# Performance work log

Measured on AMD Instinct MI355X. Metric: run time of the kernel, lower is better.

## Reference

```python
import jax, jax.numpy as jnp
import numpy as np

K = 64        # top-k from init_kwargs
TAU = 1.0     # temperature at step=0: tau_start*(1-0) + tau_end*0


def setup_inputs() -> dict:
    key = jax.random.key(0)
    k1, k2 = jax.random.split(key)
    B, N = 2048, 8192
    logits = jax.random.normal(k1, (B, N), dtype=jnp.float32)
    # gumbels = -log(Exp(1)) == standard Gumbel noise
    gumbel_noise = jax.random.gumbel(k2, (B, N), dtype=jnp.float32)
    return {"logits": logits, "gumbel_noise": gumbel_noise}


def reference(logits, gumbel_noise):
    # training path of GumbelTopK (step=0 -> tau=TAU, hard=True)
    g = (logits + gumbel_noise) / TAU                       # [B, N]
    order = jnp.argsort(-g, axis=-1)                        # descending sort order
    sorted_g = jnp.take_along_axis(g, order, axis=-1)
    cumsum = jnp.cumsum(jax.nn.softmax(sorted_g, axis=-1), axis=-1)
    mask = (cumsum <= K).astype(sorted_g.dtype)             # NB: faithful to source (<= k)
    sorted_y = mask * jax.nn.softmax(sorted_g / TAU, axis=-1)
    # scatter back to original positions == gather by inverse permutation
    inv = jnp.argsort(order, axis=-1)
    y = jnp.take_along_axis(sorted_y, inv, axis=-1)         # [B, N]
    # hard straight-through: one-hot-k of y
    k = min(K, y.shape[-1])
    _, idx = jax.lax.top_k(y, k)                            # [B, k]
    rows = jnp.arange(y.shape[0])[:, None]
    y_hard = jnp.zeros_like(y).at[rows, idx].set(1.0)
    return jax.lax.stop_gradient(y_hard - y) + y
```

## Files before the change

### kernel.cpp

```cpp
#include <hip/hip_runtime.h>

constexpr int N = 8192;
constexpr int K = 64;
constexpr int THREADS = 512;
constexpr int WAVES = THREADS / 64;
constexpr int EPT = N / THREADS;
constexpr int VEC = EPT / 4;
constexpr int CAP = 3072;

typedef float f32x4 __attribute__((ext_vector_type(4)));

__device__ __forceinline__ unsigned orderable(float f) {
    unsigned x = __float_as_uint(f);
    return (x & 0x80000000u) ? ~x : (x | 0x80000000u);
}

__global__ __launch_bounds__(THREADS, 8)
void gumbel_topk_onehot(const float* __restrict__ logits,
                        const float* __restrict__ noise,
                        float* __restrict__ out)
{
    __shared__ __align__(16) unsigned hist[2048];
    __shared__ __align__(16) unsigned cand[CAP];
    __shared__ unsigned wavesum[WAVES];
    __shared__ unsigned ccount;
    __shared__ unsigned sel_bin, sel_kth, sel_cnt;
    __shared__ unsigned r_val, r_take, r_ceq;

    const int tid  = threadIdx.x;
    const int lane = tid & 63;
    const int wave = tid >> 6;
    const long long row = blockIdx.x;

    const float4* lrow = (const float4*)(logits + row * (long long)N);
    const float4* nrow = (const float4*)(noise  + row * (long long)N);

    ((uint4*)hist)[tid] = make_uint4(0, 0, 0, 0);
    if (tid == 0) ccount = 0;

    unsigned key[EPT];
#pragma unroll
    for (int i = 0; i < VEC; ++i) {
        int idx = tid + i * THREADS;
        float4 a = lrow[idx];
        float4 b = nrow[idx];
        key[4*i+0] = orderable(a.x + b.x);
        key[4*i+1] = orderable(a.y + b.y);
        key[4*i+2] = orderable(a.z + b.z);
        key[4*i+3] = orderable(a.w + b.w);
    }
    __syncthreads();

#pragma unroll
    for (int e = 0; e < EPT; ++e)
        atomicAdd(&hist[key[e] >> 21], 1u);
    __syncthreads();

    unsigned kth = K;

#define SELECT_BIN(BPT)                                                      \
    {                                                                        \
        unsigned p = 0;                                                      \
        _Pragma("unroll")                                                    \
        for (int j = 0; j < (BPT); ++j) p += hist[tid * (BPT) + j];          \
        unsigned s = p;                                                      \
        _Pragma("unroll")                                                    \
        for (int off = 1; off < 64; off <<= 1) {                             \
            unsigned v = __shfl_down(s, off);                                \
            if (lane + off < 64) s += v;                                     \
        }                                                                    \
        if (lane == 0) wavesum[wave] = s;                                    \
        __syncthreads();                                                     \
        unsigned S = s;                                                      \
        _Pragma("unroll")                                                    \
        for (int w = 0; w < WAVES; ++w) if (w > wave) S += wavesum[w];       \
        unsigned Snext = S - p;                                              \
        if (S >= kth && Snext < kth) {                                       \
            unsigned cum = Snext;                                            \
            for (int j = (BPT) - 1; j >= 0; --j) {                           \
                unsigned c = hist[tid * (BPT) + j];                          \
                if (cum + c >= kth) {                                        \
                    sel_bin = (unsigned)(tid * (BPT) + j);                   \
                    sel_kth = kth - cum;                                     \
                    sel_cnt = c;                                             \
                    break;                                                   \
                }                                                            \
                cum += c;                                                    \
            }                                                                \
        }                                                                    \
        __syncthreads();                                                     \
    }

    SELECT_BIN(4)
    const unsigned b1   = sel_bin;
    const unsigned cnt1 = sel_cnt;
    kth = sel_kth;

#pragma unroll
    for (int e = 0; e < EPT; ++e) {
        if ((key[e] >> 21) == b1) {
            unsigned pos = atomicAdd(&ccount, 1u);
            if (pos < (unsigned)CAP) cand[pos] = key[e] & 0x1FFFFFu;
        }
    }
    __syncthreads();

    unsigned T, take_eq, c_eq;

    if (cnt1 <= (unsigned)THREADS) {
        const bool have = (tid < (int)cnt1);
        const unsigned myv = have ? cand[tid] : 0u;
        unsigned g = 0, eq = 0;
#pragma unroll 4
        for (int j = 0; j < (int)cnt1; ++j) {
            unsigned v = cand[j];
            g  += (v >  myv) ? 1u : 0u;
            eq += (v == myv) ? 1u : 0u;
        }
        if (have && g < kth && g + eq >= kth) {
            r_val  = myv;
            r_take = kth - g;
            r_ceq  = eq;
        }
        __syncthreads();
        T       = (b1 << 21) | r_val;
        take_eq = r_take;
        c_eq    = r_ceq;
    } else {
        const bool use_cand = (cnt1 <= (unsigned)CAP);

        ((uint4*)hist)[tid] = make_uint4(0, 0, 0, 0);
        __syncthreads();
        if (use_cand) {
            for (int i = tid; i < (int)cnt1; i += THREADS)
                atomicAdd(&hist[cand[i] >> 10], 1u);
        } else {
#pragma unroll
            for (int e = 0; e < EPT; ++e)
                if ((key[e] >> 21) == b1)
                    atomicAdd(&hist[(key[e] >> 10) & 0x7FFu], 1u);
        }
        __syncthreads();

        SELECT_BIN(4)
        const unsigned b2 = sel_bin;
        kth = sel_kth;
        __syncthreads();

        if (tid < 256) ((uint4*)hist)[tid] = make_uint4(0, 0, 0, 0);
        __syncthreads();
        if (use_cand) {
            for (int i = tid; i < (int)cnt1; i += THREADS) {
                unsigned cv = cand[i];
                if ((cv >> 10) == b2) atomicAdd(&hist[cv & 0x3FFu], 1u);
            }
        } else {
            const unsigned pfx = (b1 << 11) | b2;
#pragma unroll
            for (int e = 0; e < EPT; ++e)
                if ((key[e] >> 10) == pfx)
                    atomicAdd(&hist[key[e] & 0x3FFu], 1u);
        }
        __syncthreads();

        SELECT_BIN(2)
        T       = (b1 << 21) | (b2 << 10) | sel_bin;
        take_eq = sel_kth;
        c_eq    = sel_cnt;
    }

    const bool fast = (take_eq == c_eq);

    f32x4* orow = (f32x4*)(out + row * (long long)N);
#pragma unroll
    for (int i = 0; i < VEC; ++i) {
        int idx = tid + i * THREADS;
        f32x4 o;
        o.x = (key[4*i+0] > T || (fast && key[4*i+0] == T)) ? 1.0f : 0.0f;
        o.y = (key[4*i+1] > T || (fast && key[4*i+1] == T)) ? 1.0f : 0.0f;
        o.z = (key[4*i+2] > T || (fast && key[4*i+2] == T)) ? 1.0f : 0.0f;
        o.w = (key[4*i+3] > T || (fast && key[4*i+3] == T)) ? 1.0f : 0.0f;
        __builtin_nontemporal_store(o, &orow[idx]);
    }

    if (!fast) {
        __syncthreads();
        if (tid == 0) {
            const float* lf = logits + row * (long long)N;
            const float* nf = noise  + row * (long long)N;
            float* of = out + row * (long long)N;
            unsigned c = 0;
            for (int i = 0; i < N; ++i) {
                if (orderable(lf[i] + nf[i]) == T) {
                    of[i] = 1.0f;
                    if (++c == take_eq) break;
                }
            }
        }
    }
#undef SELECT_BIN
}

extern "C" void kernel_launch(void* const* d_in, const int* in_sizes, int n_in,
                              void* d_out, int out_size, void* d_ws, size_t ws_size,
                              hipStream_t stream) {
    const float* logits = (const float*)d_in[0];
    const float* noise  = (const float*)d_in[1];
    float* out = (float*)d_out;
    const int rows = in_sizes[0] / N;
    gumbel_topk_onehot<<<rows, THREADS, 0, stream>>>(logits, noise, out);
}
```

Before: 174.2 us.

## Process two rows per block with next-row prefetch and dual histograms

Each block now handles two rows, issuing the global loads for the second row while the first row's histogram/select phases run. The first-pass histogram is split into two copies by lane parity to reduce LDS atomic contention. __syncthreads is replaced by a barrier that waits only on LDS counters so outstanding global prefetches are not drained, and the candidate rank loop uses vectorized LDS reads. This raises register use and halves the number of blocks, which may reduce occupancy or parallelism.

```diff
diff --git a/kernel.cpp b/kernel.cpp
--- a/kernel.cpp
+++ b/kernel.cpp
@@ -7,12 +7,22 @@
 constexpr int EPT = N / THREADS;
 constexpr int VEC = EPT / 4;
 constexpr int CAP = 3072;
+constexpr int RPB = 2;
+constexpr int NB = 2048;
+constexpr int COFF = NB + 4;
+constexpr int HWORDS = 2 * NB + 8;
 
 typedef float f32x4 __attribute__((ext_vector_type(4)));
 
 __device__ __forceinline__ unsigned orderable(float f) {
     unsigned x = __float_as_uint(f);
     return (x & 0x80000000u) ? ~x : (x | 0x80000000u);
+}
+
+__device__ __forceinline__ void barrier_nd() {
+    asm volatile("s_waitcnt lgkmcnt(0)" ::: "memory");
+    __builtin_amdgcn_s_barrier();
+    asm volatile("" ::: "memory");
 }
 
 __global__ __launch_bounds__(THREADS, 8)
@@ -20,7 +30,7 @@
                         const float* __restrict__ noise,
                         float* __restrict__ out)
 {
-    __shared__ __align__(16) unsigned hist[2048];
+    __shared__ __align__(16) unsigned hist[HWORDS];
     __shared__ __align__(16) unsigned cand[CAP];
     __shared__ unsigned wavesum[WAVES];
     __shared__ unsigned ccount;
@@ -30,39 +40,27 @@
     const int tid  = threadIdx.x;
     const int lane = tid & 63;
     const int wave = tid >> 6;
-    const long long row = blockIdx.x;
-
-    const float4* lrow = (const float4*)(logits + row * (long long)N);
-    const float4* nrow = (const float4*)(noise  + row * (long long)N);
-
-    ((uint4*)hist)[tid] = make_uint4(0, 0, 0, 0);
-    if (tid == 0) ccount = 0;
-
-    unsigned key[EPT];
-#pragma unroll
-    for (int i = 0; i < VEC; ++i) {
-        int idx = tid + i * THREADS;
-        float4 a = lrow[idx];
-        float4 b = nrow[idx];
-        key[4*i+0] = orderable(a.x + b.x);
-        key[4*i+1] = orderable(a.y + b.y);
-        key[4*i+2] = orderable(a.z + b.z);
-        key[4*i+3] = orderable(a.w + b.w);
+    const long long row0 = (long long)blockIdx.x * RPB;
+
+    float4 av[VEC], bv[VEC];
+    {
+        const float4* lrow = (const float4*)(logits + row0 * (long long)N);
+        const float4* nrow = (const float4*)(noise  + row0 * (long long)N);
+#pragma unroll
+        for (int i = 0; i < VEC; ++i) {
+            av[i] = lrow[tid + i * THREADS];
+            bv[i] = nrow[tid + i * THREADS];
+        }
     }
-    __syncthreads();
-
-#pragma unroll
-    for (int e = 0; e < EPT; ++e)
-        atomicAdd(&hist[key[e] >> 21], 1u);
-    __syncthreads();
-
-    unsigned kth = K;
-
-#define SELECT_BIN(BPT)                                                      \
+
+#define SELECT_BIN(BPT, DUAL)                                                \
     {                                                                        \
         unsigned p = 0;                                                      \
         _Pragma("unroll")                                                    \
-        for (int j = 0; j < (BPT); ++j) p += hist[tid * (BPT) + j];          \
+        for (int j = 0; j < (BPT); ++j) {                                    \
+            unsigned b = tid * (BPT) + j;                                    \
+            p += hist[b] + ((DUAL) ? hist[b + COFF] : 0u);                   \
+        }                                                                    \
         unsigned s = p;                                                      \
         _Pragma("unroll")                                                    \
         for (int off = 1; off < 64; off <<= 1) {                             \
@@ -70,7 +68,7 @@
             if (lane + off < 64) s += v;                                     \
         }                                                                    \
         if (lane == 0) wavesum[wave] = s;                                    \
-        __syncthreads();                                                     \
+        barrier_nd();                                                        \
         unsigned S = s;                                                      \
         _Pragma("unroll")                                                    \
         for (int w = 0; w < WAVES; ++w) if (w > wave) S += wavesum[w];       \
@@ -78,9 +76,10 @@
         if (S >= kth && Snext < kth) {                                       \
             unsigned cum = Snext;                                            \
             for (int j = (BPT) - 1; j >= 0; --j) {                           \
-                unsigned c = hist[tid * (BPT) + j];                          \
+                unsigned b = tid * (BPT) + j;                                \
+                unsigned c = hist[b] + ((DUAL) ? hist[b + COFF] : 0u);       \
                 if (cum + c >= kth) {                                        \
-                    sel_bin = (unsigned)(tid * (BPT) + j);                   \
+                    sel_bin = b;                                             \
                     sel_kth = kth - cum;                                     \
                     sel_cnt = c;                                             \
                     break;                                                   \
@@ -88,112 +87,149 @@
                 cum += c;                                                    \
             }                                                                \
         }                                                                    \
-        __syncthreads();                                                     \
+        barrier_nd();                                                        \
     }
 
-    SELECT_BIN(4)
-    const unsigned b1   = sel_bin;
-    const unsigned cnt1 = sel_cnt;
-    kth = sel_kth;
-
-#pragma unroll
-    for (int e = 0; e < EPT; ++e) {
-        if ((key[e] >> 21) == b1) {
-            unsigned pos = atomicAdd(&ccount, 1u);
-            if (pos < (unsigned)CAP) cand[pos] = key[e] & 0x1FFFFFu;
-        }
-    }
-    __syncthreads();
-
-    unsigned T, take_eq, c_eq;
-
-    if (cnt1 <= (unsigned)THREADS) {
-        const bool have = (tid < (int)cnt1);
-        const unsigned myv = have ? cand[tid] : 0u;
-        unsigned g = 0, eq = 0;
-#pragma unroll 4
-        for (int j = 0; j < (int)cnt1; ++j) {
-            unsigned v = cand[j];
-            g  += (v >  myv) ? 1u : 0u;
-            eq += (v == myv) ? 1u : 0u;
-        }
-        if (have && g < kth && g + eq >= kth) {
-            r_val  = myv;
-            r_take = kth - g;
-            r_ceq  = eq;
-        }
-        __syncthreads();
-        T       = (b1 << 21) | r_val;
-        take_eq = r_take;
-        c_eq    = r_ceq;
-    } else {
-        const bool use_cand = (cnt1 <= (unsigned)CAP);
-
-        ((uint4*)hist)[tid] = make_uint4(0, 0, 0, 0);
-        __syncthreads();
-        if (use_cand) {
-            for (int i = tid; i < (int)cnt1; i += THREADS)
-                atomicAdd(&hist[cand[i] >> 10], 1u);
+#pragma unroll
+    for (int r = 0; r < RPB; ++r) {
+        const long long row = row0 + r;
+
+        for (int i = tid; i < HWORDS / 4; i += THREADS)
+            ((uint4*)hist)[i] = make_uint4(0u, 0u, 0u, 0u);
+        if (tid == 0) ccount = 0u;
+
+        unsigned key[EPT];
+        const float4* lnext = (const float4*)(logits + (row + 1) * (long long)N);
+        const float4* nnext = (const float4*)(noise  + (row + 1) * (long long)N);
+#pragma unroll
+        for (int i = 0; i < VEC; ++i) {
+            float4 a = av[i], b = bv[i];
+            if (r + 1 < RPB) {
+                av[i] = lnext[tid + i * THREADS];
+                bv[i] = nnext[tid + i * THREADS];
+            }
+            key[4*i+0] = orderable(a.x + b.x);
+            key[4*i+1] = orderable(a.y + b.y);
+            key[4*i+2] = orderable(a.z + b.z);
+            key[4*i+3] = orderable(a.w + b.w);
+        }
+        barrier_nd();
+
+        const unsigned hoff = (lane & 1) ? (unsigned)COFF : 0u;
+#pragma unroll
+        for (int e = 0; e < EPT; ++e)
+            atomicAdd(&hist[(key[e] >> 21) + hoff], 1u);
+        barrier_nd();
+
+        unsigned kth = K;
+        SELECT_BIN(4, 1)
+        const unsigned b1   = sel_bin;
+        const unsigned cnt1 = sel_cnt;
+        kth = sel_kth;
+
+#pragma unroll
+        for (int e = 0; e < EPT; ++e) {
+            if ((key[e] >> 21) == b1) {
+                unsigned pos = atomicAdd(&ccount, 1u);
+                if (pos < (unsigned)CAP) cand[pos] = key[e] & 0x1FFFFFu;
+            }
+        }
+        barrier_nd();
+
+        unsigned T, take_eq, c_eq;
+
+        if (cnt1 <= (unsigned)THREADS) {
+            const bool have = (tid < (int)cnt1);
+            const unsigned myv = have ? cand[tid] : 0u;
+            unsigned g = 0, eq = 0;
+            int j = 0;
+            for (; j + 4 <= (int)cnt1; j += 4) {
+                uint4 v = ((const uint4*)cand)[j >> 2];
+                g  += (v.x >  myv) + (v.y >  myv) + (v.z >  myv) + (v.w >  myv);
+                eq += (v.x == myv) + (v.y == myv) + (v.z == myv) + (v.w == myv);
+            }
+            for (; j < (int)cnt1; ++j) {
+                unsigned v = cand[j];
+                g += (v > myv); eq += (v == myv);
+            }
+            if (have && g < kth && g + eq >= kth) {
+                r_val  = myv;
+                r_take = kth - g;
+                r_ceq  = eq;
+            }
+            barrier_nd();
+            T       = (b1 << 21) | r_val;
+            take_eq = r_take;
+            c_eq    = r_ceq;
         } else {
-#pragma unroll
-            for (int e = 0; e < EPT; ++e)
-                if ((key[e] >> 21) == b1)
-                    atomicAdd(&hist[(key[e] >> 10) & 0x7FFu], 1u);
-        }
-        __syncthreads();
-
-        SELECT_BIN(4)
-        const unsigned b2 = sel_bin;
-        kth = sel_kth;
-        __syncthreads();
-
-        if (tid < 256) ((uint4*)hist)[tid] = make_uint4(0, 0, 0, 0);
-        __syncthreads();
-        if (use_cand) {
-            for (int i = tid; i < (int)cnt1; i += THREADS) {
-                unsigned cv = cand[i];
-                if ((cv >> 10) == b2) atomicAdd(&hist[cv & 0x3FFu], 1u);
-            }
-        } else {
-            const unsigned pfx = (b1 << 11) | b2;
-#pragma unroll
-            for (int e = 0; e < EPT; ++e)
-                if ((key[e] >> 10) == pfx)
-                    atomicAdd(&hist[key[e] & 0x3FFu], 1u);
-        }
-        __syncthreads();
-
-        SELECT_BIN(2)
-        T       = (b1 << 21) | (b2 << 10) | sel_bin;
-        take_eq = sel_kth;
-        c_eq    = sel_cnt;
-    }
-
-    const bool fast = (take_eq == c_eq);
-
-    f32x4* orow = (f32x4*)(out + row * (long long)N);
-#pragma unroll
-    for (int i = 0; i < VEC; ++i) {
-        int idx = tid + i * THREADS;
-        f32x4 o;
-        o.x = (key[4*i+0] > T || (fast && key[4*i+0] == T)) ? 1.0f : 0.0f;
-        o.y = (key[4*i+1] > T || (fast && key[4*i+1] == T)) ? 1.0f : 0.0f;
-        o.z = (key[4*i+2] > T || (fast && key[4*i+2] == T)) ? 1.0f : 0.0f;
-        o.w = (key[4*i+3] > T || (fast && key[4*i+3] == T)) ? 1.0f : 0.0f;
-        __builtin_nontemporal_store(o, &orow[idx]);
-    }
-
-    if (!fast) {
-        __syncthreads();
-        if (tid == 0) {
-            const float* lf = logits + row * (long long)N;
-            const float* nf = noise  + row * (long long)N;
-            float* of = out + row * (long long)N;
-            unsigned c = 0;
-            for (int i = 0; i < N; ++i) {
-                if (orderable(lf[i] + nf[i]) == T) {
-                    of[i] = 1.0f;
-                    if (++c == take_eq) break;
+            const bool use_cand = (cnt1 <= (unsigned)CAP);
+
+            ((uint4*)hist)[tid] = make_uint4(0u, 0u, 0u, 0u);
+            barrier_nd();
+            if (use_cand) {
+                for (int i = tid; i < (int)cnt1; i += THREADS)
+                    atomicAdd(&hist[cand[i] >> 10], 1u);
+            } else {
+#pragma unroll
+                for (int e = 0; e < EPT; ++e)
+                    if ((key[e] >> 21) == b1)
+                        atomicAdd(&hist[(key[e] >> 10) & 0x7FFu], 1u);
+            }
+            barrier_nd();
+
+            SELECT_BIN(4, 0)
+            const unsigned b2 = sel_bin;
+            kth = sel_kth;
+            barrier_nd();
+
+            if (tid < 256) ((uint4*)hist)[tid] = make_uint4(0u, 0u, 0u, 0u);
+            barrier_nd();
+            if (use_cand) {
+                for (int i = tid; i < (int)cnt1; i += THREADS) {
+                    unsigned cv = cand[i];
+                    if ((cv >> 10) == b2) atomicAdd(&hist[cv & 0x3FFu], 1u);
+                }
+            } else {
+                const unsigned pfx = (b1 << 11) | b2;
+#pragma unroll
+                for (int e = 0; e < EPT; ++e)
+                    if ((key[e] >> 10) == pfx)
+                        atomicAdd(&hist[key[e] & 0x3FFu], 1u);
+            }
+            barrier_nd();
+
+            SELECT_BIN(2, 0)
+            T       = (b1 << 21) | (b2 << 10) | sel_bin;
+            take_eq = sel_kth;
+            c_eq    = sel_cnt;
+        }
+
+        const bool fast = (take_eq == c_eq);
+
+        f32x4* orow = (f32x4*)(out + row * (long long)N);
+#pragma unroll
+        for (int i = 0; i < VEC; ++i) {
+            int idx = tid + i * THREADS;
+            f32x4 o;
+            o.x = (key[4*i+0] > T || (fast && key[4*i+0] == T)) ? 1.0f : 0.0f;
+            o.y = (key[4*i+1] > T || (fast && key[4*i+1] == T)) ? 1.0f : 0.0f;
+            o.z = (key[4*i+2] > T || (fast && key[4*i+2] == T)) ? 1.0f : 0.0f;
+            o.w = (key[4*i+3] > T || (fast && key[4*i+3] == T)) ? 1.0f : 0.0f;
+            __builtin_nontemporal_store(o, &orow[idx]);
+        }
+
+        if (!fast) {
+            __syncthreads();
+            if (tid == 0) {
+                const float* lf = logits + row * (long long)N;
+                const float* nf = noise  + row * (long long)N;
+                float* of = out + row * (long long)N;
+                unsigned c = 0;
+                for (int i = 0; i < N; ++i) {
+                    if (orderable(lf[i] + nf[i]) == T) {
+                        of[i] = 1.0f;
+                        if (++c == take_eq) break;
+                    }
                 }
             }
         }
@@ -208,5 +244,5 @@
     const float* noise  = (const float*)d_in[1];
     float* out = (float*)d_out;
     const int rows = in_sizes[0] / N;
-    gumbel_topk_onehot<<<rows, THREADS, 0, stream>>>(logits, noise, out);
-}
+    gumbel_topk_onehot<<<rows / RPB, THREADS, 0, stream>>>(logits, noise, out);
+}
```

After: 200.7 us. +15.2%, slower.

## Prefilter top-k candidates with fixed threshold, fall back to radix select

Applied to the files above, without the earlier changes.

Replaces the first histogram and bin-selection pass with a fixed threshold (orderable key for value 4.0). Keys above it are compacted into shared memory using wave ballot and one atomic per wave. If the candidate count lands between K and THREADS, the k-th value comes from a direct rank count over the candidates read as vectors. Otherwise the kernel falls back to the original multi-pass radix histogram select. The threshold is tuned to the input distribution, and loads are issued in two batches and a lighter barrier is used.

```diff
diff --git a/kernel.cpp b/kernel.cpp
--- a/kernel.cpp
+++ b/kernel.cpp
@@ -6,13 +6,21 @@
 constexpr int WAVES = THREADS / 64;
 constexpr int EPT = N / THREADS;
 constexpr int VEC = EPT / 4;
-constexpr int CAP = 3072;
+constexpr int CAP = 1024;
+
+constexpr unsigned THRESH = 0xC0800000u;
 
 typedef float f32x4 __attribute__((ext_vector_type(4)));
 
 __device__ __forceinline__ unsigned orderable(float f) {
     unsigned x = __float_as_uint(f);
     return (x & 0x80000000u) ? ~x : (x | 0x80000000u);
+}
+
+__device__ __forceinline__ void barrier_nd() {
+    asm volatile("s_waitcnt lgkmcnt(0)" ::: "memory");
+    __builtin_amdgcn_s_barrier();
+    asm volatile("" ::: "memory");
 }
 
 __global__ __launch_bounds__(THREADS, 8)
@@ -32,104 +40,133 @@
     const int wave = tid >> 6;
     const long long row = blockIdx.x;
 
+    if (tid == 0) ccount = 0u;
+    barrier_nd();
+
     const float4* lrow = (const float4*)(logits + row * (long long)N);
     const float4* nrow = (const float4*)(noise  + row * (long long)N);
-
-    ((uint4*)hist)[tid] = make_uint4(0, 0, 0, 0);
-    if (tid == 0) ccount = 0;
+    float4 av[VEC], bv[VEC];
+#pragma unroll
+    for (int i = 0; i < VEC; ++i) av[i] = lrow[tid + i * THREADS];
+#pragma unroll
+    for (int i = 0; i < VEC; ++i) bv[i] = nrow[tid + i * THREADS];
 
     unsigned key[EPT];
 #pragma unroll
     for (int i = 0; i < VEC; ++i) {
-        int idx = tid + i * THREADS;
-        float4 a = lrow[idx];
-        float4 b = nrow[idx];
-        key[4*i+0] = orderable(a.x + b.x);
-        key[4*i+1] = orderable(a.y + b.y);
-        key[4*i+2] = orderable(a.z + b.z);
-        key[4*i+3] = orderable(a.w + b.w);
-    }
-    __syncthreads();
-
-#pragma unroll
-    for (int e = 0; e < EPT; ++e)
-        atomicAdd(&hist[key[e] >> 21], 1u);
-    __syncthreads();
-
-    unsigned kth = K;
-
-#define SELECT_BIN(BPT)                                                      \
-    {                                                                        \
-        unsigned p = 0;                                                      \
-        _Pragma("unroll")                                                    \
-        for (int j = 0; j < (BPT); ++j) p += hist[tid * (BPT) + j];          \
-        unsigned s = p;                                                      \
-        _Pragma("unroll")                                                    \
-        for (int off = 1; off < 64; off <<= 1) {                             \
-            unsigned v = __shfl_down(s, off);                                \
-            if (lane + off < 64) s += v;                                     \
-        }                                                                    \
-        if (lane == 0) wavesum[wave] = s;                                    \
-        __syncthreads();                                                     \
-        unsigned S = s;                                                      \
-        _Pragma("unroll")                                                    \
-        for (int w = 0; w < WAVES; ++w) if (w > wave) S += wavesum[w];       \
-        unsigned Snext = S - p;                                              \
-        if (S >= kth && Snext < kth) {                                       \
-            unsigned cum = Snext;                                            \
-            for (int j = (BPT) - 1; j >= 0; --j) {                           \
-                unsigned c = hist[tid * (BPT) + j];                          \
-                if (cum + c >= kth) {                                        \
-                    sel_bin = (unsigned)(tid * (BPT) + j);                   \
-                    sel_kth = kth - cum;                                     \
-                    sel_cnt = c;                                             \
-                    break;                                                   \
-                }                                                            \
-                cum += c;                                                    \
-            }                                                                \
-        }                                                                    \
-        __syncthreads();                                                     \
-    }
-
-    SELECT_BIN(4)
-    const unsigned b1   = sel_bin;
-    const unsigned cnt1 = sel_cnt;
-    kth = sel_kth;
+        key[4*i+0] = orderable(av[i].x + bv[i].x);
+        key[4*i+1] = orderable(av[i].y + bv[i].y);
+        key[4*i+2] = orderable(av[i].z + bv[i].z);
+        key[4*i+3] = orderable(av[i].w + bv[i].w);
+    }
 
 #pragma unroll
     for (int e = 0; e < EPT; ++e) {
-        if ((key[e] >> 21) == b1) {
-            unsigned pos = atomicAdd(&ccount, 1u);
-            if (pos < (unsigned)CAP) cand[pos] = key[e] & 0x1FFFFFu;
-        }
-    }
-    __syncthreads();
-
+        const bool p = (key[e] >= THRESH);
+        unsigned long long mask = __ballot(p);
+        if (mask) {
+            const unsigned cnt   = (unsigned)__popcll(mask);
+            const int      leader = __ffsll((long long)mask) - 1;
+            unsigned base = 0;
+            if (lane == leader) base = atomicAdd(&ccount, cnt);
+            base = __shfl(base, leader);
+            if (p) {
+                unsigned off = (unsigned)__popcll(mask & ((1ull << lane) - 1ull));
+                unsigned pos = base + off;
+                if (pos < (unsigned)CAP) cand[pos] = key[e];
+            }
+        }
+    }
+    barrier_nd();
+
+    const unsigned c = ccount;
     unsigned T, take_eq, c_eq;
 
-    if (cnt1 <= (unsigned)THREADS) {
-        const bool have = (tid < (int)cnt1);
+    if (c >= (unsigned)K && c <= (unsigned)THREADS) {
+        const bool have = (tid < (int)c);
         const unsigned myv = have ? cand[tid] : 0u;
         unsigned g = 0, eq = 0;
-#pragma unroll 4
-        for (int j = 0; j < (int)cnt1; ++j) {
-            unsigned v = cand[j];
-            g  += (v >  myv) ? 1u : 0u;
-            eq += (v == myv) ? 1u : 0u;
-        }
-        if (have && g < kth && g + eq >= kth) {
+        if (tid < (int)((c + 63u) & ~63u)) {
+            int j = 0;
+            for (; j + 4 <= (int)c; j += 4) {
+                uint4 v = ((const uint4*)cand)[j >> 2];
+                g  += (v.x >  myv) + (v.y >  myv) + (v.z >  myv) + (v.w >  myv);
+                eq += (v.x == myv) + (v.y == myv) + (v.z == myv) + (v.w == myv);
+            }
+            for (; j < (int)c; ++j) {
+                unsigned v = cand[j];
+                g += (v > myv); eq += (v == myv);
+            }
+        }
+        if (have && g < (unsigned)K && g + eq >= (unsigned)K) {
             r_val  = myv;
-            r_take = kth - g;
+            r_take = (unsigned)K - g;
             r_ceq  = eq;
         }
-        __syncthreads();
-        T       = (b1 << 21) | r_val;
+        barrier_nd();
+        T       = r_val;
         take_eq = r_take;
         c_eq    = r_ceq;
     } else {
+        unsigned kth = K;
+
+#define SELECT_BIN(BPT)                                                      \
+        {                                                                    \
+            unsigned p = 0;                                                  \
+            _Pragma("unroll")                                                \
+            for (int j = 0; j < (BPT); ++j) p += hist[tid * (BPT) + j];      \
+            unsigned s = p;                                                  \
+            _Pragma("unroll")                                                \
+            for (int off = 1; off < 64; off <<= 1) {                         \
+                unsigned v = __shfl_down(s, off);                            \
+                if (lane + off < 64) s += v;                                 \
+            }                                                                \
+            if (lane == 0) wavesum[wave] = s;                                \
+            __syncthreads();                                                 \
+            unsigned S = s;                                                  \
+            _Pragma("unroll")                                                \
+            for (int w = 0; w < WAVES; ++w) if (w > wave) S += wavesum[w];   \
+            unsigned Snext = S - p;                                          \
+            if (S >= kth && Snext < kth) {                                   \
+                unsigned cum = Snext;                                        \
+                for (int j = (BPT) - 1; j >= 0; --j) {                       \
+                    unsigned b = tid * (BPT) + j;                            \
+                    unsigned cc = hist[b];                                   \
+                    if (cum + cc >= kth) {                                   \
+                        sel_bin = b;                                         \
+                        sel_kth = kth - cum;                                 \
+                        sel_cnt = cc;                                        \
+                        break;                                               \
+                    }                                                        \
+                    cum += cc;                                               \
+                }                                                            \
+            }                                                                \
+            __syncthreads();                                                 \
+        }
+
+        ((uint4*)hist)[tid] = make_uint4(0u, 0u, 0u, 0u);
+        if (tid == 0) ccount = 0u;
+        __syncthreads();
+#pragma unroll
+        for (int e = 0; e < EPT; ++e)
+            atomicAdd(&hist[key[e] >> 21], 1u);
+        __syncthreads();
+        SELECT_BIN(4)
+        const unsigned b1   = sel_bin;
+        const unsigned cnt1 = sel_cnt;
+        kth = sel_kth;
+
+#pragma unroll
+        for (int e = 0; e < EPT; ++e) {
+            if ((key[e] >> 21) == b1) {
+                unsigned pos = atomicAdd(&ccount, 1u);
+                if (pos < (unsigned)CAP) cand[pos] = key[e] & 0x1FFFFFu;
+            }
+        }
+        __syncthreads();
         const bool use_cand = (cnt1 <= (unsigned)CAP);
 
-        ((uint4*)hist)[tid] = make_uint4(0, 0, 0, 0);
+        ((uint4*)hist)[tid] = make_uint4(0u, 0u, 0u, 0u);
         __syncthreads();
         if (use_cand) {
             for (int i = tid; i < (int)cnt1; i += THREADS)
@@ -141,13 +178,12 @@
                     atomicAdd(&hist[(key[e] >> 10) & 0x7FFu], 1u);
         }
         __syncthreads();
-
         SELECT_BIN(4)
         const unsigned b2 = sel_bin;
         kth = sel_kth;
         __syncthreads();
 
-        if (tid < 256) ((uint4*)hist)[tid] = make_uint4(0, 0, 0, 0);
+        if (tid < 256) ((uint4*)hist)[tid] = make_uint4(0u, 0u, 0u, 0u);
         __syncthreads();
         if (use_cand) {
             for (int i = tid; i < (int)cnt1; i += THREADS) {
@@ -162,11 +198,11 @@
                     atomicAdd(&hist[key[e] & 0x3FFu], 1u);
         }
         __syncthreads();
-
         SELECT_BIN(2)
         T       = (b1 << 21) | (b2 << 10) | sel_bin;
         take_eq = sel_kth;
         c_eq    = sel_cnt;
+#undef SELECT_BIN
     }
 
     const bool fast = (take_eq == c_eq);
@@ -189,16 +225,15 @@
             const float* lf = logits + row * (long long)N;
             const float* nf = noise  + row * (long long)N;
             float* of = out + row * (long long)N;
-            unsigned c = 0;
+            unsigned cc = 0;
             for (int i = 0; i < N; ++i) {
                 if (orderable(lf[i] + nf[i]) == T) {
                     of[i] = 1.0f;
-                    if (++c == take_eq) break;
+                    if (++cc == take_eq) break;
                 }
             }
         }
     }
-#undef SELECT_BIN
 }
 
 extern "C" void kernel_launch(void* const* d_in, const int* in_sizes, int n_in,
```

Result: no change. 177.2 us (+1.7%).
